# Kernel tuning notes

Hardware: AMD Instinct MI355X
Metric: run time of the kernel (lower is better)

The kernel has to match this reference:

```python
import jax, jax.numpy as jnp
import numpy as np

B, L, IN, H, E = 64, 255, 32, 256, 128
PAD = (L - 1) // 2
DN = ('NCH', 'OIH', 'NCH')


def setup_inputs() -> dict:
    ks = jax.random.split(jax.random.key(0), 10)
    r = lambda k, shp, s=0.05: jax.random.normal(k, shp, dtype=jnp.float32) * s
    return {
        's': jax.random.normal(ks[0], (B, L, IN), dtype=jnp.float32),
        'conv1_w': r(ks[1], (H, IN, L)),
        'conv1_b': r(ks[2], (H,)),
        'bn_gamma': jnp.ones((H,), jnp.float32),
        'bn_beta': jnp.zeros((H,), jnp.float32),
        'conv2_w': r(ks[3], (E, H, L)),
        'conv2_b': r(ks[4], (E,)),
        'pw1': r(ks[5], (E, H, L)),   # stacked Linear(L, H) weights, one per channel
        'pb1': r(ks[6], (E, H)),
        'pw2': r(ks[7], (E, 2, H)),   # stacked Linear(H, 2) weights
        'pb2': r(ks[8], (E, 2)),
    }


def reference(s, conv1_w, conv1_b, bn_gamma, bn_beta, conv2_w, conv2_b, pw1, pb1, pw2, pb2):
    x = jnp.transpose(s, (0, 2, 1))  # (B, IN, T)
    h = jax.lax.conv_general_dilated(x, conv1_w, (1,), [(PAD, PAD)], dimension_numbers=DN)
    h = jax.nn.relu(h + conv1_b[None, :, None])
    # BatchNorm1d in training mode: biased batch stats over (N, T)
    mean = h.mean(axis=(0, 2), keepdims=True)
    var = ((h - mean) ** 2).mean(axis=(0, 2), keepdims=True)
    h = (h - mean) * jax.lax.rsqrt(var + 1e-5) * bn_gamma[None, :, None] + bn_beta[None, :, None]
    z = jax.lax.conv_general_dilated(h, conv2_w, (1,), [(PAD, PAD)], dimension_numbers=DN)
    z = jnp.transpose(z + conv2_b[None, :, None], (0, 2, 1))  # (B, T, E)

    rf = jnp.fft.rfft(z, axis=1)                 # (B, F, E), F = L//2 + 1 == E
    power = jnp.abs(rf)[:, :, 1:] ** 2           # faithful channel-axis slice -> (B, F, E-1)
    freq_bins = jnp.fft.rfftfreq(L)[1:]          # (F-1,) == (E-1,)
    frequency = jnp.sum(freq_bins * power, axis=1) / jnp.sum(power, axis=1)  # (B, E-1)
    amplitude = 2.0 * jnp.sqrt(jnp.sum(power, axis=1)) / L                    # (B, E-1)
    offset = rf.real[:, :, 0] / L                                              # (B, E)

    # batched per-channel 2-layer MLP (replaces Python loop over embedding_dim)
    hmid = jax.nn.relu(jnp.einsum('btc,cht->bch', z, pw1) + pb1[None])  # (B, E, H)
    ang = jnp.einsum('bch,coh->bco', hmid, pw2) + pb2[None]             # (B, E, 2)
    phase = jnp.arctan2(ang[:, :, 1], ang[:, :, 0])                     # (B, E)
    return (amplitude, phase, frequency, offset)
```

## Files before the change

kernel.cpp:

```cpp
#include <hip/hip_runtime.h>
#include <math.h>

#define TB   64
#define TT   255
#define TIN  32
#define NH   256
#define NE   128
#define NK   255
#define NPAD 127

#define NF    384
#define NBINS 193
#define NFC   386
#define FCP   416
#define HCH   64

typedef __attribute__((ext_vector_type(8))) short short8;
typedef __attribute__((ext_vector_type(4))) float float4v;

#define WSB_WP1  0u
#define WSB_Z    0u
#define WSB_HFU  8388608u
#define WSB_HMID 8388608u
#define WSB_W2S  25165824u
#define WSB_HSP  37814272u
#define WSB_BIH  37814272u
#define WSB_BIL  38027264u
#define WSB_BIM  38240256u
#define WSB_ZSP  44138496u
#define WSB_BDH  56786944u
#define WSB_BDL  56984576u
#define WSB_BDM  57182208u
#define WSB_BWH  57379840u
#define WSB_BWL  57577472u
#define WSB_BWM  57775104u
#define WSB_D1   57972736u
#define WSB_BN   57974528u

#define O_AMP   0u
#define O_PHASE 8128u
#define O_FREQ  16320u
#define O_OFF   24448u

static __device__ __forceinline__ unsigned short f2bf(float f) {
  unsigned int u = __float_as_uint(f);
  unsigned int r = (u + 0x7FFFu + ((u >> 16) & 1u)) >> 16;
  return (unsigned short)r;
}
static __device__ __forceinline__ float bf2f(unsigned short s) {
  return __uint_as_float(((unsigned int)s) << 16);
}
static __device__ __forceinline__ short8 as_s8(uint4 v) {
  union { uint4 u; short8 s; } c; c.u = v; return c.s;
}

static __device__ __forceinline__ void split3(float x, unsigned short& h,
                                              unsigned short& l, unsigned short& m2) {
  h = f2bf(x);
  float r1 = x - bf2f(h);
  l = f2bf(r1);
// ... 41 lines not shown
  put_hi(U2, r, p, pm);
}
static __device__ __forceinline__ short8 frag(const unsigned short* __restrict__ lds,
                                              int row, int quad, int part) {
  return *(const short8*)&lds[row * 64 + (((quad ^ (part << 2)) ^ (row & 7)) << 3)];
}
#define MF(a, b, c) __builtin_amdgcn_mfma_f32_16x16x32_bf16((a), (b), (c), 0, 0, 0)
#define MF6(accv, ahv, alv, a2v, bhv, blv, b2v) do {                              \
    accv = MF(ahv, bhv, accv);                                                    \
    accv = MF(ahv, blv, accv);                                                    \
    accv = MF(alv, bhv, accv);                                                    \
    accv = MF(alv, blv, accv);                                                    \
    accv = MF(ahv, b2v, accv);                                                    \
    accv = MF(a2v, bhv, accv);                                                    \
  } while (0)
#define MF5(accv, ahv, alv, a2v, bhv, blv) do {                                   \
    accv = MF(ahv, bhv, accv);                                                    \
    accv = MF(ahv, blv, accv);                                                    \
    accv = MF(alv, bhv, accv);                                                    \
    accv = MF(alv, blv, accv);                                                    \
    accv = MF(a2v, bhv, accv);                                                    \
  } while (0)

__global__ __launch_bounds__(256) void bn_zero_k(float* __restrict__ bn) {
  bn[threadIdx.x] = 0.f;
  bn[256 + threadIdx.x] = 0.f;
}

__global__ __launch_bounds__(256) void basis_init_k(
    unsigned int* __restrict__ bdh, unsigned int* __restrict__ bdl,
    unsigned int* __restrict__ bdm, unsigned int* __restrict__ bwh,
    unsigned int* __restrict__ bwl, unsigned int* __restrict__ bwm) {
  __shared__ float sv[2][256];
  const int m = blockIdx.x;
  const int t = threadIdx.x;
  const int f = m >> 1, im = m & 1;
  const float C = 6.28318530717958647692f / 384.f;
  int r1 = (f * t) % 384;
  float th1 = C * (float)r1;
  sv[0][t] = (t == 255) ? 0.f : (im ? -sinf(th1) : cosf(th1));
  int a = f * (t - 127);
  int r2 = a % 384; if (r2 < 0) r2 += 384;
  float th2 = C * (float)r2;
  sv[1][t] = (t == 255) ? 0.f : (im ? sinf(th2) : cosf(th2));
  __syncthreads();
  const int which = t >> 7, j = t & 127;
  unsigned int ph, pl, pm;
  split_pack2(sv[which][2 * j], sv[which][2 * j + 1], ph, pl, pm);
  size_t off = (size_t)m * 128 + j;
  if (which == 0) { bdh[off] = ph; bdl[off] = pl; bdm[off] = pm; }
  else            { bwh[off] = ph; bwl[off] = pl; bwm[off] = pm; }
}

__global__ __launch_bounds__(256) void d1_k(float* __restrict__ d1) {
  const int fc = blockIdx.x * 256 + threadIdx.x;
  if (fc >= NFC) return;
  const int f = fc >> 1, im = fc & 1;
  const float C = 6.28318530717958647692f / 384.f;
  float s = 0.f;
  int r = 0;
  for (int t = 0; t < TT; ++t) {
    float th = C * (float)r;
    s += im ? -sinf(th) : cosf(th);
    r += f; if (r >= 384) r -= 384;
  }
  d1[fc] = s;
}

__global__ __launch_bounds__(256) void basis_bi_k(
    unsigned int* __restrict__ bih, unsigned int* __restrict__ bil,
    unsigned int* __restrict__ bim) {
  const int kp = blockIdx.x;
  const int t = threadIdx.x;
  float x0 = 0.f, x1 = 0.f;
  if (kp < NBINS) {
    const int f = kp;
    const float C = 6.28318530717958647692f / 384.f;
    int r1 = (f * t) % 384;
    float th = C * (float)r1;
    float wgt = ((f == 0 || f == 192) ? 1.f : 2.f) * (1.f / 384.f);
    x0 = cosf(th) * wgt;
    x1 = -sinf(th) * wgt;
  }
  unsigned int ph, pl, pm;
  split_pack2(x0, x1, ph, pl, pm);
  size_t off = (size_t)kp * 256 + t;
  bih[off] = ph; bil[off] = pl; bim[off] = pm;
}

__global__ __launch_bounds__(256) void pack1_k(const float* __restrict__ w1,
                                               unsigned int* __restrict__ wp1u) {
  __shared__ float tile[512][33];
  const int et = blockIdx.x, kc = blockIdx.y;
  const int kk0 = kc * 32, cnt = min(32, NK - kk0);
  const int tid = threadIdx.x;
  for (int idx = tid; idx < 512 * 32; idx += 256) {
    int row = idx >> 5, kl = idx & 31;
    if (kl < cnt) {
      int e_l = row >> 5, i_l = row & 31;
      tile[row][kl] = w1[(size_t)((et * 16 + e_l) * TIN + i_l) * NK + kk0 + kl];
    }
  }
  __syncthreads();
  const int lane = tid >> 2, jp = (tid & 3) * 2;
  const int row0 = (lane & 15) * 32 + (lane >> 4) * 8 + jp;
  for (int kl = 0; kl < cnt; ++kl) {
    float w0 = tile[row0][kl], w1v = tile[row0 + 1][kl];
    unsigned short h0 = f2bf(w0), h1 = f2bf(w1v);
    unsigned short l0 = f2bf(w0 - bf2f(h0)), l1 = f2bf(w1v - bf2f(h1));
    size_t base = (size_t)(kk0 + kl) * 8192 + et * 512 + tid;
    wp1u[base] = (unsigned int)h0 | ((unsigned int)h1 << 16);
    wp1u[base + 256] = (unsigned int)l0 | ((unsigned int)l1 << 16);
  }
}

#define C1_ROWS 384
__global__ __launch_bounds__(256, 2) void conv1_mfma(
    const float* __restrict__ s, const unsigned int* __restrict__ wp1u,
    const float* __restrict__ b1v, unsigned int* __restrict__ hfu,
    float* __restrict__ bn) {
  __shared__ __align__(16) unsigned short Alds[C1_ROWS * 64];
  const int th = blockIdx.x & 1, chg = blockIdx.x >> 1, b = blockIdx.y;
  const int tid = threadIdx.x, lane = tid & 63, wv = tid >> 6;
  const int quad = lane >> 4, l15 = lane & 15;
  const int tg = wv & 1, eg = wv >> 1;
  unsigned int* Au = (unsigned int*)Alds;

  for (int idx = tid; idx < C1_ROWS * 16; idx += 256) {
    int r = idx >> 4, p = idx & 15;
    int t = th * 128 + r - NPAD;
    float v0 = 0.f, v1 = 0.f;
    if (t >= 0 && t < TT) {
      const float* sp = &s[(size_t)(b * TT + t) * TIN + p * 2];
      v0 = sp[0]; v1 = sp[1];
    }
// ... 66 lines not shown
          unsigned short vh = f2bf(v);
          unsigned short vl = f2bf(v - bf2f(vh));
          hfu[(size_t)(b * 256 + t) * NH + ch] =
              (unsigned int)vh | ((unsigned int)vl << 16);
          s1[ni] += v; s2[ni] += v * v;
        }
      }
    }
  }
#pragma unroll
  for (int ni = 0; ni < 2; ++ni) {
    s1[ni] += __shfl_xor(s1[ni], 16);
    s1[ni] += __shfl_xor(s1[ni], 32);
    s2[ni] += __shfl_xor(s2[ni], 16);
    s2[ni] += __shfl_xor(s2[ni], 32);
    if (quad == 0) {
      int ch = chg * 64 + (eg * 2 + ni) * 16 + l15;
      atomicAdd(&bn[ch], s1[ni]);
      atomicAdd(&bn[256 + ch], s2[ni]);
    }
  }
#undef LOADB1
#undef MSTEP1
}

__global__ __launch_bounds__(256) void bn_final_k(const float* __restrict__ gamma,
                                                  const float* __restrict__ beta,
                                                  float* __restrict__ bn) {
  const int h = threadIdx.x;
  const float inv = 1.0f / (TB * TT);
  float m = bn[h] * inv;
  float var = bn[256 + h] * inv - m * m;
  float sc = gamma[h] / sqrtf(var + 1e-5f);
  bn[512 + h] = sc;
  bn[768 + h] = beta[h] - m * sc;
}


#define LOAD_A_PLANES(PH, PL, PM) do {                                            \
    if (fcA < NFC) {                                                              \
      size_t ab = (size_t)fcA * 128 + (k0 >> 1) + hfA * 8;                        \
      uint4 h0v = *(const uint4*)(PH + ab), h1v = *(const uint4*)(PH + ab + 4);   \
      uint4 l0v = *(const uint4*)(PL + ab), l1v = *(const uint4*)(PL + ab + 4);   \
      uint4 m0v = *(const uint4*)(PM + ab), m1v = *(const uint4*)(PM + ab + 4);   \
      _Pragma("unroll")                                                           \
      for (int q = 0; q < 4; ++q) {                                               \
        put_hi(Au, rA, hfA * 8 + q, ((const unsigned int*)&h0v)[q]);              \
        put_hi(Au, rA, hfA * 8 + 4 + q, ((const unsigned int*)&h1v)[q]);          \
        put_lo(Au, rA, hfA * 8 + q, ((const unsigned int*)&l0v)[q]);              \
        put_lo(Au, rA, hfA * 8 + 4 + q, ((const unsigned int*)&l1v)[q]);          \
        put_hi(A2u, rA, hfA * 8 + q, ((const unsigned int*)&m0v)[q]);             \
        put_hi(A2u, rA, hfA * 8 + 4 + q, ((const unsigned int*)&m1v)[q]);         \
      }                                                                           \
    } else {                                                                      \
      _Pragma("unroll")                                                           \
      for (int q = 0; q < 8; ++q) {                                               \
        put_hi(Au, rA, hfA * 8 + q, 0u);                                          \
        put_lo(Au, rA, hfA * 8 + q, 0u);                                          \
        put_hi(A2u, rA, hfA * 8 + q, 0u);                                         \
      }                                                                           \
    }                                                                             \
  } while (0)

__global__ __launch_bounds__(256, 2) void w2prep_mfma(
    const float* __restrict__ w2, const unsigned int* __restrict__ bwh,
    const unsigned int* __restrict__ bwl, const unsigned int* __restrict__ bwm,
    float* __restrict__ W, int h0c) {
  __shared__ __align__(16) unsigned short Alds[128 * 64];
  __shared__ __align__(16) unsigned short A2lds[128 * 64];
  __shared__ __align__(16) unsigned short Blds[128 * 64];
  __shared__ __align__(16) unsigned short B2lds[128 * 64];
  const int n0 = blockIdx.x * 128, m0 = blockIdx.y * 128;
  const int tid = threadIdx.x, lane = tid & 63, wv = tid >> 6;
  const int quad = lane >> 4, l15 = lane & 15;
  const int wm = wv >> 1, wn = wv & 1;
  unsigned int* Au = (unsigned int*)Alds;
  unsigned int* A2u = (unsigned int*)A2lds;
  unsigned int* Bu = (unsigned int*)Blds;
  unsigned int* B2u = (unsigned int*)B2lds;

  float4v acc[4][4];
#pragma unroll
  for (int i = 0; i < 4; ++i)
#pragma unroll
    for (int j = 0; j < 4; ++j) acc[i][j] = (float4v)(0.f);

  const int rA = tid >> 1, hfA = tid & 1;
  const int fcA = m0 + rA;
  const int lane8 = tid & 7, rsub = tid >> 3;

  for (int kk = 0; kk < 8; ++kk) {
    const int k0 = kk * 32;
    if (kk) __syncthreads();
    LOAD_A_PLANES(bwh, bwl, bwm);
#pragma unroll
    for (int pass = 0; pass < 4; ++pass) {
      int row = pass * 32 + rsub;
      int e = (n0 + row) >> 6, hl = (n0 + row) & 63;
      const float* src = w2 + ((size_t)(e * NH + h0c + hl)) * NK;
      int kb = k0 + lane8 * 4;
      float f0 = (kb < NK) ? src[kb] : 0.f;
      float f1 = (kb + 1 < NK) ? src[kb + 1] : 0.f;
      float f2 = (kb + 2 < NK) ? src[kb + 2] : 0.f;
      float f3 = (kb + 3 < NK) ? src[kb + 3] : 0.f;
      stage2_3(Bu, B2u, row, lane8 * 2, f0, f1);
      stage2_3(Bu, B2u, row, lane8 * 2 + 1, f2, f3);
    }
    __syncthreads();
    short8 bh[4], bl[4], b2[4];
#pragma unroll
    for (int ni = 0; ni < 4; ++ni) {
      int rb = wn * 64 + ni * 16 + l15;
      bh[ni] = frag(Blds, rb, quad, 0);
      bl[ni] = frag(Blds, rb, quad, 1);
      b2[ni] = frag(B2lds, rb, quad, 0);
    }
#pragma unroll
    for (int mi = 0; mi < 4; ++mi) {
      int ra = wm * 64 + mi * 16 + l15;
      short8 ah = frag(Alds, ra, quad, 0);
      short8 al = frag(Alds, ra, quad, 1);
      short8 a2 = frag(A2lds, ra, quad, 0);
#pragma unroll
      for (int ni = 0; ni < 4; ++ni) MF6(acc[mi][ni], ah, al, a2, bh[ni], bl[ni], b2[ni]);
    }
  }
#pragma unroll
  for (int mi = 0; mi < 4; ++mi) {
    int fc0 = m0 + wm * 64 + mi * 16 + quad * 4;
#pragma unroll
    for (int ni = 0; ni < 4; ++ni) {
      int n = n0 + wn * 64 + ni * 16 + l15;
#pragma unroll
      for (int r = 0; r < 4; ++r) {
        if (fc0 + r < NFC) W[(size_t)(fc0 + r) * 8192 + n] = acc[mi][ni][r];
      }
    }
  }
}

__global__ __launch_bounds__(256, 2) void dftH_mfma(
    const unsigned int* __restrict__ hfu, const float* __restrict__ bn,
    const unsigned int* __restrict__ bdh, const unsigned int* __restrict__ bdl,
    const unsigned int* __restrict__ bdm, const float* __restrict__ d1,
    float* __restrict__ H, int h0c) {
  __shared__ __align__(16) unsigned short Alds[128 * 64];
  __shared__ __align__(16) unsigned short A2lds[128 * 64];
  __shared__ __align__(16) unsigned short Blds[64 * 64];
  const int b = blockIdx.x, m0 = blockIdx.y * 128;
  const int tid = threadIdx.x, lane = tid & 63, wv = tid >> 6;
  const int quad = lane >> 4, l15 = lane & 15;
  const int wm = wv >> 1, wn = wv & 1;
  const int hl = tid & 63, g = tid >> 6;
  unsigned int* Au = (unsigned int*)Alds;
  unsigned int* A2u = (unsigned int*)A2lds;
  unsigned int* Bu = (unsigned int*)Blds;

  float4v acc[4][2];
#pragma unroll
  for (int i = 0; i < 4; ++i)
#pragma unroll
    for (int j = 0; j < 2; ++j) acc[i][j] = (float4v)(0.f);

  const int rA = tid >> 1, hfA = tid & 1;
  const int fcA = m0 + rA;

  for (int kk = 0; kk < 8; ++kk) {
    const int k0 = kk * 32;
    if (kk) __syncthreads();
    LOAD_A_PLANES(bdh, bdl, bdm);
#pragma unroll
    for (int j = 0; j < 4; ++j) {
      int tp = g * 4 + j;
      int t0 = k0 + tp * 2;
      unsigned int u0 = (t0 < TT)
          ? hfu[(size_t)(b * 256 + t0) * NH + h0c + hl] : 0u;
      unsigned int u1 = (t0 + 1 < TT)
          ? hfu[(size_t)(b * 256 + t0 + 1) * NH + h0c + hl] : 0u;
      unsigned int hp = (u0 & 0xFFFFu) | ((u1 & 0xFFFFu) << 16);
      unsigned int lp = (u0 >> 16) | (u1 & 0xFFFF0000u);
      put_hi(Bu, hl, tp, hp);
      put_lo(Bu, hl, tp, lp);
    }
    __syncthreads();
    short8 bh[2], bl[2];
#pragma unroll
    for (int ni = 0; ni < 2; ++ni) {
      int rb = wn * 32 + ni * 16 + l15;
      bh[ni] = frag(Blds, rb, quad, 0);
      bl[ni] = frag(Blds, rb, quad, 1);
    }
#pragma unroll
    for (int mi = 0; mi < 4; ++mi) {
      int ra = wm * 64 + mi * 16 + l15;
      short8 ah = frag(Alds, ra, quad, 0);
      short8 al = frag(Alds, ra, quad, 1);
      short8 a2 = frag(A2lds, ra, quad, 0);
#pragma unroll
      for (int ni = 0; ni < 2; ++ni) MF5(acc[mi][ni], ah, al, a2, bh[ni], bl[ni]);
    }
  }
#pragma unroll
  for (int mi = 0; mi < 4; ++mi) {
    int fc0 = m0 + wm * 64 + mi * 16 + quad * 4;
#pragma unroll
    for (int ni = 0; ni < 2; ++ni) {
      int hli = wn * 32 + ni * 16 + l15;
      float scv = bn[512 + h0c + hli];
      float shv = bn[768 + h0c + hli];
#pragma unroll
      for (int r = 0; r < 4; ++r) {
        int fc = fc0 + r;
        if (fc < NFC)
          H[(size_t)fc * 4096 + b * 64 + hli] = scv * acc[mi][ni][r] + shv * d1[fc];
      }
    }
  }
}

__global__ __launch_bounds__(256, 2) void fgemm_mfma(
    const float* __restrict__ H, const float* __restrict__ W,
    float* __restrict__ zsp, int first) {
  __shared__ __align__(16) unsigned short Alds[64 * 64];
  __shared__ __align__(16) unsigned short A2lds[64 * 64];
  __shared__ __align__(16) unsigned short Blds[128 * 64];
  __shared__ __align__(16) unsigned short B2lds[128 * 64];
  const int ri = blockIdx.x, f = blockIdx.y;
  const int tid = threadIdx.x, lane = tid & 63, wv = tid >> 6;
  const int quad = lane >> 4, l15 = lane & 15;
  const int wm = wv >> 1, wn = wv & 1;
  unsigned int* Au = (unsigned int*)Alds;
  unsigned int* A2u = (unsigned int*)A2lds;
  unsigned int* Bu = (unsigned int*)Blds;
  unsigned int* B2u = (unsigned int*)B2lds;

  float4v acc[2][4];
#pragma unroll
  for (int i = 0; i < 2; ++i)
#pragma unroll
    for (int j = 0; j < 4; ++j) acc[i][j] = (float4v)(0.f);

  const int rA = tid >> 2, qA = tid & 3;
  const int rB = tid >> 1, hB = tid & 1;

  for (int kk = 0; kk < 4; ++kk) {
    const int ca = kk >> 1;
    const int hb = (kk & 1) * 32;
    if (kk) __syncthreads();
    {
      float va[8];
      const float4* s4 = (const float4*)(H + (size_t)(2 * f + ca) * 4096 + rA * 64 + hb + qA * 8);
      *(float4*)(va + 0) = s4[0]; *(float4*)(va + 4) = s4[1];
      stage8_3(Au, A2u, rA, qA * 4, va);
    }
    {
      const int cb = ri ^ (kk >> 1);
      const int neg = (ri == 0 && kk >= 2);
      float vb[16];
      const float4* s4 = (const float4*)(W + (size_t)(2 * f + cb) * 8192 + rB * 64 + hb + hB * 16);
      *(float4*)(vb + 0) = s4[0]; *(float4*)(vb + 4) = s4[1];
      *(float4*)(vb + 8) = s4[2]; *(float4*)(vb + 12) = s4[3];
      if (neg) {
#pragma unroll
        for (int q = 0; q < 16; ++q) vb[q] = -vb[q];
      }
      stage8_3(Bu, B2u, rB, hB * 8, vb);
      stage8_3(Bu, B2u, rB, hB * 8 + 4, vb + 8);
    }
    __syncthreads();
    short8 bh[4], bl[4], b2[4];
#pragma unroll
    for (int ni = 0; ni < 4; ++ni) {
      int rb = wn * 64 + ni * 16 + l15;
      bh[ni] = frag(Blds, rb, quad, 0);
      bl[ni] = frag(Blds, rb, quad, 1);
      b2[ni] = frag(B2lds, rb, quad, 0);
    }
#pragma unroll
    for (int mi = 0; mi < 2; ++mi) {
      int ra = wm * 32 + mi * 16 + l15;
      short8 ah = frag(Alds, ra, quad, 0);
      short8 al = frag(Alds, ra, quad, 1);
      short8 a2 = frag(A2lds, ra, quad, 0);
#pragma unroll
      for (int ni = 0; ni < 4; ++ni) MF6(acc[mi][ni], ah, al, a2, bh[ni], bl[ni], b2[ni]);
    }
  }
  float* Z = zsp + (size_t)(2 * f + ri) * 8192;
#pragma unroll
  for (int mi = 0; mi < 2; ++mi) {
#pragma unroll
    for (int ni = 0; ni < 4; ++ni) {
      int e = wn * 64 + ni * 16 + l15;
#pragma unroll
      for (int r = 0; r < 4; ++r) {
        int b = wm * 32 + mi * 16 + quad * 4 + r;
        size_t off = (size_t)b * 128 + e;
        if (first) Z[off] = acc[mi][ni][r];
        else       Z[off] += acc[mi][ni][r];
      }
    }
  }
}

__global__ __launch_bounds__(256, 2) void idft_mfma(
    const float* __restrict__ zsp, const unsigned int* __restrict__ bih,
    const unsigned int* __restrict__ bil, const unsigned int* __restrict__ bim,
    const float* __restrict__ b2, float* __restrict__ z) {
  __shared__ __align__(16) unsigned short Alds[128 * 64];
  __shared__ __align__(16) unsigned short A2lds[128 * 64];
  __shared__ __align__(16) unsigned short Blds[64 * 64];
  __shared__ __align__(16) unsigned short B2lds[64 * 64];
  const int n0 = blockIdx.x * 64, m0 = blockIdx.y * 128;
  const int tid = threadIdx.x, lane = tid & 63, wv = tid >> 6;
  const int quad = lane >> 4, l15 = lane & 15;
  const int wm = wv >> 1, wn = wv & 1;
  const int tl = tid & 63, g = tid >> 6;
  unsigned int* Au = (unsigned int*)Alds;
  unsigned int* A2u = (unsigned int*)A2lds;
  unsigned int* Bu = (unsigned int*)Blds;
  unsigned int* B2u = (unsigned int*)B2lds;

  float4v acc[4][2];
#pragma unroll
  for (int i = 0; i < 4; ++i)
#pragma unroll
    for (int j = 0; j < 2; ++j) acc[i][j] = (float4v)(0.f);

  for (int kk = 0; kk < 13; ++kk) {
    const int k0 = kk * 32;
    if (kk) __syncthreads();
#pragma unroll
    for (int i = 0; i < 8; ++i) {
      int combo = i * 4 + g;
      int tp = combo >> 1, beh = combo & 1;
      int fc0 = k0 + tp * 2;
      int row = beh * 64 + lane;
      float v0 = (fc0 < NFC) ? zsp[(size_t)fc0 * 8192 + m0 + row] : 0.f;
      float v1 = (fc0 + 1 < NFC) ? zsp[(size_t)(fc0 + 1) * 8192 + m0 + row] : 0.f;
      stage2_3(Au, A2u, row, tp, v0, v1);
    }
#pragma unroll
    for (int j = 0; j < 4; ++j) {
      int tp = g * 4 + j;
      size_t off = (size_t)((k0 >> 1) + tp) * 256 + n0 + tl;
      put_hi(Bu, tl, tp, bih[off]);
      put_lo(Bu, tl, tp, bil[off]);
      put_hi(B2u, tl, tp, bim[off]);
    }
    __syncthreads();
    short8 bh[2], bl[2], b2f[2];
#pragma unroll
    for (int ni = 0; ni < 2; ++ni) {
      int rb = wn * 32 + ni * 16 + l15;
      bh[ni] = frag(Blds, rb, quad, 0);
      bl[ni] = frag(Blds, rb, quad, 1);
      b2f[ni] = frag(B2lds, rb, quad, 0);
    }
#pragma unroll
    for (int mi = 0; mi < 4; ++mi) {
      int ra = wm * 64 + mi * 16 + l15;
      short8 ah = frag(Alds, ra, quad, 0);
      short8 al = frag(Alds, ra, quad, 1);
      short8 a2 = frag(A2lds, ra, quad, 0);
#pragma unroll
      for (int ni = 0; ni < 2; ++ni) MF6(acc[mi][ni], ah, al, a2, bh[ni], bl[ni], b2f[ni]);
    }
  }
#pragma unroll
  for (int mi = 0; mi < 4; ++mi) {
#pragma unroll
// ... 35 lines not shown
      float4 zv = *(const float4*)&zl[t * 68 + b4 * 4];
      float4 pv = *(const float4*)&pl[t * 68 + h4 * 4];
      float zz[4] = {zv.x, zv.y, zv.z, zv.w};
      float pp[4] = {pv.x, pv.y, pv.z, pv.w};
#pragma unroll
      for (int a = 0; a < 4; ++a)
#pragma unroll
        for (int bb = 0; bb < 4; ++bb) acc[a][bb] = fmaf(pp[a], zz[bb], acc[a][bb]);
    }
  }
#pragma unroll
  for (int a = 0; a < 4; ++a) {
    int hh = h0 + h4 * 4 + a;
    float bias = pb1[c * NH + hh];
#pragma unroll
    for (int bb = 0; bb < 4; ++bb) {
      int bidx = b4 * 4 + bb;
      float v = acc[a][bb] + bias;
      hmid[(size_t)(bidx * NE + c) * NH + hh] = fmaxf(v, 0.f);
    }
  }
}

__global__ __launch_bounds__(256) void mlp2_k(const float* __restrict__ hmid,
                                              const float* __restrict__ pw2,
                                              const float* __restrict__ pb2,
                                              float* __restrict__ out) {
  const int tid = threadIdx.x, lane = tid & 63, wv = tid >> 6;
  const int p = blockIdx.x * 4 + wv;
  const int b = p >> 7, c = p & 127;
  const float4 hv = *(const float4*)&hmid[(size_t)(b * NE + c) * NH + lane * 4];
  const float4 p0 = *(const float4*)&pw2[(size_t)(c * 2 + 0) * NH + lane * 4];
  const float4 p1 = *(const float4*)&pw2[(size_t)(c * 2 + 1) * NH + lane * 4];
  float s0 = hv.x * p0.x + hv.y * p0.y + hv.z * p0.z + hv.w * p0.w;
  float s1 = hv.x * p1.x + hv.y * p1.y + hv.z * p1.z + hv.w * p1.w;
#pragma unroll
  for (int off = 32; off; off >>= 1) {
    s0 += __shfl_down(s0, off);
    s1 += __shfl_down(s1, off);
  }
  if (lane == 0) {
    float a0 = s0 + pb2[c * 2 + 0];
    float a1 = s1 + pb2[c * 2 + 1];
    out[O_PHASE + b * NE + c] = atan2f(a1, a0);
  }
}

__global__ __launch_bounds__(256) void amp_k(const float* __restrict__ z,
                                             float* __restrict__ out) {
  const int tid = threadIdx.x, lane = tid & 63, wv = tid >> 6;
  const int b = blockIdx.x, c = blockIdx.y * 4 + wv;
  const float* row = z + (size_t)(b * NE + c) * TT;
  float s1 = 0.f, s2 = 0.f;
  for (int idx = lane; idx < TT; idx += 64) {
    float v = row[idx];
    s1 += v; s2 += v * v;
  }
#pragma unroll
  for (int off = 32; off; off >>= 1) {
    s1 += __shfl_down(s1, off);
    s2 += __shfl_down(s2, off);
  }
  if (lane == 0 && c >= 1) {
    float P = 0.5f * (255.f * s2 + s1 * s1);
    out[O_AMP + b * 127 + (c - 1)] = 2.f * sqrtf(P) / 255.f;
    out[O_FREQ + b * 127 + (c - 1)] = (float)c / 255.f;
  }
}

__global__ __launch_bounds__(128) void offset_k(const float* __restrict__ z,
                                                float* __restrict__ out) {
  __shared__ float zr[TT];
  __shared__ float ct[TT];
  const int b = blockIdx.x, tid = threadIdx.x;
  for (int idx = tid; idx < TT; idx += 128) {
    zr[idx] = z[(size_t)(b * NE + 0) * TT + idx];
    ct[idx] = cosf(6.283185307179586f * (float)idx / 255.f);
  }
  __syncthreads();
  const int f = tid;
  float s = 0.f;
  int m = 0;
  for (int t = 0; t < TT; ++t) {
    s += zr[t] * ct[m];
    m += f; if (m >= TT) m -= TT;
  }
  out[O_OFF + b * NE + f] = s / 255.f;
}

extern "C" void kernel_launch(void* const* d_in, const int* in_sizes, int n_in,
                              void* d_out, int out_size, void* d_ws, size_t ws_size,
                              hipStream_t stream) {
  (void)in_sizes; (void)n_in; (void)out_size; (void)ws_size;
  const float* s       = (const float*)d_in[0];
  const float* conv1_w = (const float*)d_in[1];
  const float* conv1_b = (const float*)d_in[2];
  const float* bn_g    = (const float*)d_in[3];
  const float* bn_b    = (const float*)d_in[4];
  const float* conv2_w = (const float*)d_in[5];
  const float* conv2_b = (const float*)d_in[6];
  const float* pw1     = (const float*)d_in[7];
  const float* pb1     = (const float*)d_in[8];
  const float* pw2     = (const float*)d_in[9];
  const float* pb2     = (const float*)d_in[10];
  float* out = (float*)d_out;
  char* ws   = (char*)d_ws;

  unsigned int* wp1u = (unsigned int*)(ws + WSB_WP1);
  float* z    = (float*)(ws + WSB_Z);
  unsigned int* hfu = (unsigned int*)(ws + WSB_HFU);
  float* hmid = (float*)(ws + WSB_HMID);
  float* W2s  = (float*)(ws + WSB_W2S);
  float* Hs   = (float*)(ws + WSB_HSP);
  float* zsp  = (float*)(ws + WSB_ZSP);
  unsigned int* bdh = (unsigned int*)(ws + WSB_BDH);
  unsigned int* bdl = (unsigned int*)(ws + WSB_BDL);
  unsigned int* bdm = (unsigned int*)(ws + WSB_BDM);
  unsigned int* bwh = (unsigned int*)(ws + WSB_BWH);
  unsigned int* bwl = (unsigned int*)(ws + WSB_BWL);
  unsigned int* bwm = (unsigned int*)(ws + WSB_BWM);
  unsigned int* bih = (unsigned int*)(ws + WSB_BIH);
  unsigned int* bil = (unsigned int*)(ws + WSB_BIL);
  unsigned int* bim = (unsigned int*)(ws + WSB_BIM);
  float* d1 = (float*)(ws + WSB_D1);
  float* bn = (float*)(ws + WSB_BN);

  bn_zero_k<<<1, 256, 0, stream>>>(bn);
  basis_init_k<<<NFC, 256, 0, stream>>>(bdh, bdl, bdm, bwh, bwl, bwm);
  d1_k<<<2, 256, 0, stream>>>(d1);
  pack1_k<<<dim3(16, 8), 256, 0, stream>>>(conv1_w, wp1u);

  conv1_mfma<<<dim3(8, TB), 256, 0, stream>>>(s, wp1u, conv1_b, hfu, bn);
  bn_final_k<<<1, 256, 0, stream>>>(bn_g, bn_b, bn);

  for (int c = 0; c < 4; ++c) {
    w2prep_mfma<<<dim3(64, 4), 256, 0, stream>>>(conv2_w, bwh, bwl, bwm, W2s, c * HCH);
    dftH_mfma<<<dim3(64, 4), 256, 0, stream>>>(hfu, bn, bdh, bdl, bdm, d1, Hs, c * HCH);
    fgemm_mfma<<<dim3(2, NBINS), 256, 0, stream>>>(Hs, W2s, zsp, c == 0 ? 1 : 0);
  }
  basis_bi_k<<<208, 256, 0, stream>>>(bih, bil, bim);
  idft_mfma<<<dim3(4, 64), 256, 0, stream>>>(zsp, bih, bil, bim, conv2_b, z);

  mlp1_k<<<dim3(4, NE), 256, 0, stream>>>(z, pw1, pb1, hmid);
  mlp2_k<<<TB * NE / 4, 256, 0, stream>>>(hmid, pw2, pb2, out);
  amp_k<<<dim3(TB, 32), 256, 0, stream>>>(z, out);
  offset_k<<<TB, 128, 0, stream>>>(z, out);
}
```

Baseline: 729.4 us.

## Merge setup and tail kernels, run DFT-H once, rechunk the conv2 frequency GEMM

Folds the init kernels (bn zero, basis, d1, weight packing) into one launch and the three output kernels into one tail kernel. The BN finalize step moves into dftH, which now runs once over all 256 channels into a larger H buffer instead of four times. The w2prep/fgemm loop drops from four 64-channel chunks to three chunks of 96/96/64. The inverse-DFT basis is rebuilt on the fly from the forward basis planes, so its separate init kernel goes away. Launch count falls, at the cost of a bigger workspace and a non-power-of-two index split.

```diff
diff --git a/kernel.cpp b/kernel.cpp
--- a/kernel.cpp
+++ b/kernel.cpp
@@ -13,29 +13,26 @@
 #define NBINS 193
 #define NFC   386
 #define FCP   416
-#define HCH   64
+#define W2ROW 12288
+#define HSROW 16384
 
 typedef __attribute__((ext_vector_type(8))) short short8;
 typedef __attribute__((ext_vector_type(4))) float float4v;
 
-#define WSB_WP1  0u
+#define WSB_W2S  0u
 #define WSB_Z    0u
 #define WSB_HFU  8388608u
 #define WSB_HMID 8388608u
-#define WSB_W2S  25165824u
-#define WSB_HSP  37814272u
-#define WSB_BIH  37814272u
-#define WSB_BIL  38027264u
-#define WSB_BIM  38240256u
-#define WSB_ZSP  44138496u
-#define WSB_BDH  56786944u
-#define WSB_BDL  56984576u
-#define WSB_BDM  57182208u
-#define WSB_BWH  57379840u
-#define WSB_BWL  57577472u
-#define WSB_BWM  57775104u
-#define WSB_D1   57972736u
-#define WSB_BN   57974528u
+#define WSB_ZSP  18972672u
+#define WSB_HS   31621120u
+#define WSB_BDH  56918144u
+#define WSB_BDL  57115776u
+#define WSB_BDM  57313408u
+#define WSB_BWH  57511040u
+#define WSB_BWL  57708672u
+#define WSB_BWM  57906304u
+#define WSB_D1   58103936u
+#define WSB_BN   58105984u
 
 #define O_AMP   0u
 #define O_PHASE 8128u
@@ -123,95 +120,77 @@
     accv = MF(a2v, bhv, accv);                                                    \
   } while (0)
 
-__global__ __launch_bounds__(256) void bn_zero_k(float* __restrict__ bn) {
-  bn[threadIdx.x] = 0.f;
-  bn[256 + threadIdx.x] = 0.f;
-}
-
-__global__ __launch_bounds__(256) void basis_init_k(
+__global__ __launch_bounds__(256) void init_k(
+    const float* __restrict__ w1, unsigned int* __restrict__ wp1u,
     unsigned int* __restrict__ bdh, unsigned int* __restrict__ bdl,
     unsigned int* __restrict__ bdm, unsigned int* __restrict__ bwh,
-    unsigned int* __restrict__ bwl, unsigned int* __restrict__ bwm) {
-  __shared__ float sv[2][256];
-  const int m = blockIdx.x;
-  const int t = threadIdx.x;
-  const int f = m >> 1, im = m & 1;
-  const float C = 6.28318530717958647692f / 384.f;
-  int r1 = (f * t) % 384;
-  float th1 = C * (float)r1;
-  sv[0][t] = (t == 255) ? 0.f : (im ? -sinf(th1) : cosf(th1));
-  int a = f * (t - 127);
-  int r2 = a % 384; if (r2 < 0) r2 += 384;
-  float th2 = C * (float)r2;
-  sv[1][t] = (t == 255) ? 0.f : (im ? sinf(th2) : cosf(th2));
-  __syncthreads();
-  const int which = t >> 7, j = t & 127;
-  unsigned int ph, pl, pm;
-  split_pack2(sv[which][2 * j], sv[which][2 * j + 1], ph, pl, pm);
-  size_t off = (size_t)m * 128 + j;
-  if (which == 0) { bdh[off] = ph; bdl[off] = pl; bdm[off] = pm; }
-  else            { bwh[off] = ph; bwl[off] = pl; bwm[off] = pm; }
-}
-
-__global__ __launch_bounds__(256) void d1_k(float* __restrict__ d1) {
-  const int fc = blockIdx.x * 256 + threadIdx.x;
-  if (fc >= NFC) return;
-  const int f = fc >> 1, im = fc & 1;
-  const float C = 6.28318530717958647692f / 384.f;
-  float s = 0.f;
-  int r = 0;
-  for (int t = 0; t < TT; ++t) {
-    float th = C * (float)r;
-    s += im ? -sinf(th) : cosf(th);
-    r += f; if (r >= 384) r -= 384;
-  }
-  d1[fc] = s;
-}
-
-__global__ __launch_bounds__(256) void basis_bi_k(
-    unsigned int* __restrict__ bih, unsigned int* __restrict__ bil,
-    unsigned int* __restrict__ bim) {
-  const int kp = blockIdx.x;
-  const int t = threadIdx.x;
-  float x0 = 0.f, x1 = 0.f;
-  if (kp < NBINS) {
-    const int f = kp;
+    unsigned int* __restrict__ bwl, unsigned int* __restrict__ bwm,
+    float* __restrict__ d1, float* __restrict__ bn) {
+  __shared__ float tile[512][33];
+  const int bid = blockIdx.x, tid = threadIdx.x;
+  if (bid == 0) {
+    bn[tid] = 0.f;
+    bn[256 + tid] = 0.f;
+    return;
+  }
+  if (bid < 387) {
+    float* sv = (float*)tile;
+    const int m = bid - 1, t = tid;
+    const int f = m >> 1, im = m & 1;
     const float C = 6.28318530717958647692f / 384.f;
     int r1 = (f * t) % 384;
-    float th = C * (float)r1;
-    float wgt = ((f == 0 || f == 192) ? 1.f : 2.f) * (1.f / 384.f);
-    x0 = cosf(th) * wgt;
-    x1 = -sinf(th) * wgt;
-  }
-  unsigned int ph, pl, pm;
-  split_pack2(x0, x1, ph, pl, pm);
-  size_t off = (size_t)kp * 256 + t;
-  bih[off] = ph; bil[off] = pl; bim[off] = pm;
-}
-
-__global__ __launch_bounds__(256) void pack1_k(const float* __restrict__ w1,
-                                               unsigned int* __restrict__ wp1u) {
-  __shared__ float tile[512][33];
-  const int et = blockIdx.x, kc = blockIdx.y;
-  const int kk0 = kc * 32, cnt = min(32, NK - kk0);
-  const int tid = threadIdx.x;
-  for (int idx = tid; idx < 512 * 32; idx += 256) {
-    int row = idx >> 5, kl = idx & 31;
-    if (kl < cnt) {
-      int e_l = row >> 5, i_l = row & 31;
-      tile[row][kl] = w1[(size_t)((et * 16 + e_l) * TIN + i_l) * NK + kk0 + kl];
-    }
-  }
-  __syncthreads();
-  const int lane = tid >> 2, jp = (tid & 3) * 2;
-  const int row0 = (lane & 15) * 32 + (lane >> 4) * 8 + jp;
-  for (int kl = 0; kl < cnt; ++kl) {
-    float w0 = tile[row0][kl], w1v = tile[row0 + 1][kl];
-    unsigned short h0 = f2bf(w0), h1 = f2bf(w1v);
-    unsigned short l0 = f2bf(w0 - bf2f(h0)), l1 = f2bf(w1v - bf2f(h1));
-    size_t base = (size_t)(kk0 + kl) * 8192 + et * 512 + tid;
-    wp1u[base] = (unsigned int)h0 | ((unsigned int)h1 << 16);
-    wp1u[base + 256] = (unsigned int)l0 | ((unsigned int)l1 << 16);
+    float th1 = C * (float)r1;
+    sv[t] = (t == 255) ? 0.f : (im ? -sinf(th1) : cosf(th1));
+    int a = f * (t - 127);
+    int r2 = a % 384; if (r2 < 0) r2 += 384;
+    float th2 = C * (float)r2;
+    sv[256 + t] = (t == 255) ? 0.f : (im ? sinf(th2) : cosf(th2));
+    __syncthreads();
+    const int which = t >> 7, j = t & 127;
+    unsigned int ph, pl, pm;
+    split_pack2(sv[which * 256 + 2 * j], sv[which * 256 + 2 * j + 1], ph, pl, pm);
+    size_t off = (size_t)m * 128 + j;
+    if (which == 0) { bdh[off] = ph; bdl[off] = pl; bdm[off] = pm; }
+    else            { bwh[off] = ph; bwl[off] = pl; bwm[off] = pm; }
+    return;
+  }
+  if (bid < 389) {
+    const int fc = (bid - 387) * 256 + tid;
+    if (fc >= NFC) return;
+    const int f = fc >> 1, im = fc & 1;
+    const float C = 6.28318530717958647692f / 384.f;
+    float s = 0.f;
+    int r = 0;
+    for (int t = 0; t < TT; ++t) {
+      float th = C * (float)r;
+      s += im ? -sinf(th) : cosf(th);
+      r += f; if (r >= 384) r -= 384;
+    }
+    d1[fc] = s;
+    return;
+  }
+  {
+    const int q = bid - 389;
+    const int et = q >> 3, kc = q & 7;
+    const int kk0 = kc * 32, cnt = min(32, NK - kk0);
+    for (int idx = tid; idx < 512 * 32; idx += 256) {
+      int row = idx >> 5, kl = idx & 31;
+      if (kl < cnt) {
+        int e_l = row >> 5, i_l = row & 31;
+        tile[row][kl] = w1[(size_t)((et * 16 + e_l) * TIN + i_l) * NK + kk0 + kl];
+      }
+    }
+    __syncthreads();
+    const int lane = tid >> 2, jp = (tid & 3) * 2;
+    const int row0 = (lane & 15) * 32 + (lane >> 4) * 8 + jp;
+    for (int kl = 0; kl < cnt; ++kl) {
+      float w0 = tile[row0][kl], w1v = tile[row0 + 1][kl];
+      unsigned short h0 = f2bf(w0), h1 = f2bf(w1v);
+      unsigned short l0 = f2bf(w0 - bf2f(h0)), l1 = f2bf(w1v - bf2f(h1));
+      size_t base = (size_t)(kk0 + kl) * 8192 + et * 512 + tid;
+      wp1u[base] = (unsigned int)h0 | ((unsigned int)h1 << 16);
+      wp1u[base + 256] = (unsigned int)l0 | ((unsigned int)l1 << 16);
+    }
   }
 }
 
@@ -324,18 +303,6 @@
   }
 #undef LOADB1
 #undef MSTEP1
-}
-
-__global__ __launch_bounds__(256) void bn_final_k(const float* __restrict__ gamma,
-                                                  const float* __restrict__ beta,
-                                                  float* __restrict__ bn) {
-  const int h = threadIdx.x;
-  const float inv = 1.0f / (TB * TT);
-  float m = bn[h] * inv;
-  float var = bn[256 + h] * inv - m * m;
-  float sc = gamma[h] / sqrtf(var + 1e-5f);
-  bn[512 + h] = sc;
-  bn[768 + h] = beta[h] - m * sc;
 }
 
 
@@ -364,10 +331,102 @@
     }                                                                             \
   } while (0)
 
+__global__ __launch_bounds__(256, 2) void dftH_mfma(
+    const unsigned int* __restrict__ hfu, const float* __restrict__ bn,
+    const float* __restrict__ gamma, const float* __restrict__ beta,
+    const unsigned int* __restrict__ bdh, const unsigned int* __restrict__ bdl,
+    const unsigned int* __restrict__ bdm, const float* __restrict__ d1,
+    float* __restrict__ H) {
+  __shared__ __align__(16) unsigned short Alds[128 * 64];
+  __shared__ __align__(16) unsigned short A2lds[128 * 64];
+  __shared__ __align__(16) unsigned short Blds[64 * 64];
+  __shared__ float scs[64], shs[64];
+  const int b = blockIdx.x, m0 = blockIdx.y * 128, h0c = blockIdx.z * 64;
+  const int tid = threadIdx.x, lane = tid & 63, wv = tid >> 6;
+  const int quad = lane >> 4, l15 = lane & 15;
+  const int wm = wv >> 1, wn = wv & 1;
+  const int hl = tid & 63, g = tid >> 6;
+  unsigned int* Au = (unsigned int*)Alds;
+  unsigned int* A2u = (unsigned int*)A2lds;
+  unsigned int* Bu = (unsigned int*)Blds;
+
+  if (tid < 64) {
+    int h = h0c + tid;
+    const float inv = 1.0f / (TB * TT);
+    float m = bn[h] * inv;
+    float var = bn[256 + h] * inv - m * m;
+    float sc = gamma[h] / sqrtf(var + 1e-5f);
+    scs[tid] = sc;
+    shs[tid] = beta[h] - m * sc;
+  }
+
+  float4v acc[4][2];
+#pragma unroll
+  for (int i = 0; i < 4; ++i)
+#pragma unroll
+    for (int j = 0; j < 2; ++j) acc[i][j] = (float4v)(0.f);
+
+  const int rA = tid >> 1, hfA = tid & 1;
+  const int fcA = m0 + rA;
+
+  for (int kk = 0; kk < 8; ++kk) {
+    const int k0 = kk * 32;
+    if (kk) __syncthreads();
+    LOAD_A_PLANES(bdh, bdl, bdm);
+#pragma unroll
+    for (int j = 0; j < 4; ++j) {
+      int tp = g * 4 + j;
+      int t0 = k0 + tp * 2;
+      unsigned int u0 = (t0 < TT)
+          ? hfu[(size_t)(b * 256 + t0) * NH + h0c + hl] : 0u;
+      unsigned int u1 = (t0 + 1 < TT)
+          ? hfu[(size_t)(b * 256 + t0 + 1) * NH + h0c + hl] : 0u;
+      unsigned int hp = (u0 & 0xFFFFu) | ((u1 & 0xFFFFu) << 16);
+      unsigned int lp = (u0 >> 16) | (u1 & 0xFFFF0000u);
+      put_hi(Bu, hl, tp, hp);
+      put_lo(Bu, hl, tp, lp);
+    }
+    __syncthreads();
+    short8 bh[2], bl[2];
+#pragma unroll
+    for (int ni = 0; ni < 2; ++ni) {
+      int rb = wn * 32 + ni * 16 + l15;
+      bh[ni] = frag(Blds, rb, quad, 0);
+      bl[ni] = frag(Blds, rb, quad, 1);
+    }
+#pragma unroll
+    for (int mi = 0; mi < 4; ++mi) {
+      int ra = wm * 64 + mi * 16 + l15;
+      short8 ah = frag(Alds, ra, quad, 0);
+      short8 al = frag(Alds, ra, quad, 1);
+      short8 a2 = frag(A2lds, ra, quad, 0);
+#pragma unroll
+      for (int ni = 0; ni < 2; ++ni) MF5(acc[mi][ni], ah, al, a2, bh[ni], bl[ni]);
+    }
+  }
+#pragma unroll
+  for (int mi = 0; mi < 4; ++mi) {
+    int fc0 = m0 + wm * 64 + mi * 16 + quad * 4;
+#pragma unroll
+    for (int ni = 0; ni < 2; ++ni) {
+      int hli = wn * 32 + ni * 16 + l15;
+      float scv = scs[hli];
+      float shv = shs[hli];
+#pragma unroll
+      for (int r = 0; r < 4; ++r) {
+        int fc = fc0 + r;
+        if (fc < NFC)
+          H[(size_t)fc * HSROW + b * 256 + h0c + hli] =
+              scv * acc[mi][ni][r] + shv * d1[fc];
+      }
+    }
+  }
+}
+
 __global__ __launch_bounds__(256, 2) void w2prep_mfma(
     const float* __restrict__ w2, const unsigned int* __restrict__ bwh,
     const unsigned int* __restrict__ bwl, const unsigned int* __restrict__ bwm,
-    float* __restrict__ W, int h0c) {
+    float* __restrict__ W, int h0c, int hcnt) {
   __shared__ __align__(16) unsigned short Alds[128 * 64];
   __shared__ __align__(16) unsigned short A2lds[128 * 64];
   __shared__ __align__(16) unsigned short Blds[128 * 64];
@@ -398,13 +457,15 @@
 #pragma unroll
     for (int pass = 0; pass < 4; ++pass) {
       int row = pass * 32 + rsub;
-      int e = (n0 + row) >> 6, hl = (n0 + row) & 63;
+      int n = n0 + row;
+      int e = n / 96, hl = n - e * 96;
+      int ok = (hl < hcnt);
       const float* src = w2 + ((size_t)(e * NH + h0c + hl)) * NK;
       int kb = k0 + lane8 * 4;
-      float f0 = (kb < NK) ? src[kb] : 0.f;
-      float f1 = (kb + 1 < NK) ? src[kb + 1] : 0.f;
-      float f2 = (kb + 2 < NK) ? src[kb + 2] : 0.f;
-      float f3 = (kb + 3 < NK) ? src[kb + 3] : 0.f;
+      float f0 = (ok && kb < NK) ? src[kb] : 0.f;
+      float f1 = (ok && kb + 1 < NK) ? src[kb + 1] : 0.f;
+      float f2 = (ok && kb + 2 < NK) ? src[kb + 2] : 0.f;
+      float f3 = (ok && kb + 3 < NK) ? src[kb + 3] : 0.f;
       stage2_3(Bu, B2u, row, lane8 * 2, f0, f1);
       stage2_3(Bu, B2u, row, lane8 * 2 + 1, f2, f3);
     }
@@ -435,86 +496,7 @@
       int n = n0 + wn * 64 + ni * 16 + l15;
 #pragma unroll
       for (int r = 0; r < 4; ++r) {
-        if (fc0 + r < NFC) W[(size_t)(fc0 + r) * 8192 + n] = acc[mi][ni][r];
-      }
-    }
-  }
-}
-
-__global__ __launch_bounds__(256, 2) void dftH_mfma(
-    const unsigned int* __restrict__ hfu, const float* __restrict__ bn,
-    const unsigned int* __restrict__ bdh, const unsigned int* __restrict__ bdl,
-    const unsigned int* __restrict__ bdm, const float* __restrict__ d1,
-    float* __restrict__ H, int h0c) {
-  __shared__ __align__(16) unsigned short Alds[128 * 64];
-  __shared__ __align__(16) unsigned short A2lds[128 * 64];
-  __shared__ __align__(16) unsigned short Blds[64 * 64];
-  const int b = blockIdx.x, m0 = blockIdx.y * 128;
-  const int tid = threadIdx.x, lane = tid & 63, wv = tid >> 6;
-  const int quad = lane >> 4, l15 = lane & 15;
-  const int wm = wv >> 1, wn = wv & 1;
-  const int hl = tid & 63, g = tid >> 6;
-  unsigned int* Au = (unsigned int*)Alds;
-  unsigned int* A2u = (unsigned int*)A2lds;
-  unsigned int* Bu = (unsigned int*)Blds;
-
-  float4v acc[4][2];
-#pragma unroll
-  for (int i = 0; i < 4; ++i)
-#pragma unroll
-    for (int j = 0; j < 2; ++j) acc[i][j] = (float4v)(0.f);
-
-  const int rA = tid >> 1, hfA = tid & 1;
-  const int fcA = m0 + rA;
-
-  for (int kk = 0; kk < 8; ++kk) {
-    const int k0 = kk * 32;
-    if (kk) __syncthreads();
-    LOAD_A_PLANES(bdh, bdl, bdm);
-#pragma unroll
-    for (int j = 0; j < 4; ++j) {
-      int tp = g * 4 + j;
-      int t0 = k0 + tp * 2;
-      unsigned int u0 = (t0 < TT)
-          ? hfu[(size_t)(b * 256 + t0) * NH + h0c + hl] : 0u;
-      unsigned int u1 = (t0 + 1 < TT)
-          ? hfu[(size_t)(b * 256 + t0 + 1) * NH + h0c + hl] : 0u;
-      unsigned int hp = (u0 & 0xFFFFu) | ((u1 & 0xFFFFu) << 16);
-      unsigned int lp = (u0 >> 16) | (u1 & 0xFFFF0000u);
-      put_hi(Bu, hl, tp, hp);
-      put_lo(Bu, hl, tp, lp);
-    }
-    __syncthreads();
-    short8 bh[2], bl[2];
-#pragma unroll
-    for (int ni = 0; ni < 2; ++ni) {
-      int rb = wn * 32 + ni * 16 + l15;
-      bh[ni] = frag(Blds, rb, quad, 0);
-      bl[ni] = frag(Blds, rb, quad, 1);
-    }
-#pragma unroll
-    for (int mi = 0; mi < 4; ++mi) {
-      int ra = wm * 64 + mi * 16 + l15;
-      short8 ah = frag(Alds, ra, quad, 0);
-      short8 al = frag(Alds, ra, quad, 1);
-      short8 a2 = frag(A2lds, ra, quad, 0);
-#pragma unroll
-      for (int ni = 0; ni < 2; ++ni) MF5(acc[mi][ni], ah, al, a2, bh[ni], bl[ni]);
-    }
-  }
-#pragma unroll
-  for (int mi = 0; mi < 4; ++mi) {
-    int fc0 = m0 + wm * 64 + mi * 16 + quad * 4;
-#pragma unroll
-    for (int ni = 0; ni < 2; ++ni) {
-      int hli = wn * 32 + ni * 16 + l15;
-      float scv = bn[512 + h0c + hli];
-      float shv = bn[768 + h0c + hli];
-#pragma unroll
-      for (int r = 0; r < 4; ++r) {
-        int fc = fc0 + r;
-        if (fc < NFC)
-          H[(size_t)fc * 4096 + b * 64 + hli] = scv * acc[mi][ni][r] + shv * d1[fc];
+        if (fc0 + r < NFC) W[(size_t)(fc0 + r) * W2ROW + n] = acc[mi][ni][r];
       }
     }
   }
@@ -522,7 +504,7 @@
 
 __global__ __launch_bounds__(256, 2) void fgemm_mfma(
     const float* __restrict__ H, const float* __restrict__ W,
-    float* __restrict__ zsp, int first) {
+    float* __restrict__ zsp, int c96, int nks, int first) {
   __shared__ __align__(16) unsigned short Alds[64 * 64];
   __shared__ __align__(16) unsigned short A2lds[64 * 64];
   __shared__ __align__(16) unsigned short Blds[128 * 64];
@@ -545,21 +527,23 @@
   const int rA = tid >> 2, qA = tid & 3;
   const int rB = tid >> 1, hB = tid & 1;
 
-  for (int kk = 0; kk < 4; ++kk) {
-    const int ca = kk >> 1;
-    const int hb = (kk & 1) * 32;
-    if (kk) __syncthreads();
+  for (int ph = 0; ph < 2 * nks; ++ph) {
+    const int ca = (ph >= nks) ? 1 : 0;
+    const int hsub = (ph - ca * nks) * 32;
+    if (ph) __syncthreads();
     {
       float va[8];
-      const float4* s4 = (const float4*)(H + (size_t)(2 * f + ca) * 4096 + rA * 64 + hb + qA * 8);
+      const float4* s4 = (const float4*)(H + (size_t)(2 * f + ca) * HSROW +
+                                         rA * 256 + c96 + hsub + qA * 8);
       *(float4*)(va + 0) = s4[0]; *(float4*)(va + 4) = s4[1];
       stage8_3(Au, A2u, rA, qA * 4, va);
     }
     {
-      const int cb = ri ^ (kk >> 1);
-      const int neg = (ri == 0 && kk >= 2);
+      const int cb = ri ^ ca;
+      const int neg = (ri == 0 && ca == 1);
       float vb[16];
-      const float4* s4 = (const float4*)(W + (size_t)(2 * f + cb) * 8192 + rB * 64 + hb + hB * 16);
+      const float4* s4 = (const float4*)(W + (size_t)(2 * f + cb) * W2ROW +
+                                         rB * 96 + hsub + hB * 16);
       *(float4*)(vb + 0) = s4[0]; *(float4*)(vb + 4) = s4[1];
       *(float4*)(vb + 8) = s4[2]; *(float4*)(vb + 12) = s4[3];
       if (neg) {
@@ -606,8 +590,8 @@
 }
 
 __global__ __launch_bounds__(256, 2) void idft_mfma(
-    const float* __restrict__ zsp, const unsigned int* __restrict__ bih,
-    const unsigned int* __restrict__ bil, const unsigned int* __restrict__ bim,
+    const float* __restrict__ zsp, const unsigned int* __restrict__ bdh,
+    const unsigned int* __restrict__ bdl, const unsigned int* __restrict__ bdm,
     const float* __restrict__ b2, float* __restrict__ z) {
   __shared__ __align__(16) unsigned short Alds[128 * 64];
   __shared__ __align__(16) unsigned short A2lds[128 * 64];
@@ -645,10 +629,22 @@
 #pragma unroll
     for (int j = 0; j < 4; ++j) {
       int tp = g * 4 + j;
-      size_t off = (size_t)((k0 >> 1) + tp) * 256 + n0 + tl;
-      put_hi(Bu, tl, tp, bih[off]);
-      put_lo(Bu, tl, tp, bil[off]);
-      put_hi(B2u, tl, tp, bim[off]);
+      int fc0 = k0 + tp * 2;
+      float x0 = 0.f, x1 = 0.f;
+      if (fc0 < NFC) {
+        int fq = fc0 >> 1;
+        float sw = ((fq == 0 || fq == 192) ? 1.f : 2.f) * (1.f / 384.f);
+        int t = n0 + tl;
+        int pi = t >> 1, hs = (t & 1) * 16;
+        size_t o0 = (size_t)fc0 * 128 + pi, o1 = o0 + 128;
+        x0 = (bf2f((unsigned short)(bdh[o0] >> hs)) +
+              bf2f((unsigned short)(bdl[o0] >> hs)) +
+              bf2f((unsigned short)(bdm[o0] >> hs))) * sw;
+        x1 = (bf2f((unsigned short)(bdh[o1] >> hs)) +
+              bf2f((unsigned short)(bdl[o1] >> hs)) +
+              bf2f((unsigned short)(bdm[o1] >> hs))) * sw;
+      }
+      stage2_3(Bu, B2u, tl, tp, x0, x1);
     }
     __syncthreads();
     short8 bh[2], bl[2], b2f[2];
@@ -730,70 +726,74 @@
   }
 }
 
-__global__ __launch_bounds__(256) void mlp2_k(const float* __restrict__ hmid,
+__global__ __launch_bounds__(256) void tail_k(const float* __restrict__ hmid,
                                               const float* __restrict__ pw2,
                                               const float* __restrict__ pb2,
+                                              const float* __restrict__ z,
                                               float* __restrict__ out) {
-  const int tid = threadIdx.x, lane = tid & 63, wv = tid >> 6;
-  const int p = blockIdx.x * 4 + wv;
-  const int b = p >> 7, c = p & 127;
-  const float4 hv = *(const float4*)&hmid[(size_t)(b * NE + c) * NH + lane * 4];
-  const float4 p0 = *(const float4*)&pw2[(size_t)(c * 2 + 0) * NH + lane * 4];
-  const float4 p1 = *(const float4*)&pw2[(size_t)(c * 2 + 1) * NH + lane * 4];
-  float s0 = hv.x * p0.x + hv.y * p0.y + hv.z * p0.z + hv.w * p0.w;
-  float s1 = hv.x * p1.x + hv.y * p1.y + hv.z * p1.z + hv.w * p1.w;
-#pragma unroll
-  for (int off = 32; off; off >>= 1) {
-    s0 += __shfl_down(s0, off);
-    s1 += __shfl_down(s1, off);
-  }
-  if (lane == 0) {
-    float a0 = s0 + pb2[c * 2 + 0];
-    float a1 = s1 + pb2[c * 2 + 1];
-    out[O_PHASE + b * NE + c] = atan2f(a1, a0);
-  }
-}
-
-__global__ __launch_bounds__(256) void amp_k(const float* __restrict__ z,
-                                             float* __restrict__ out) {
-  const int tid = threadIdx.x, lane = tid & 63, wv = tid >> 6;
-  const int b = blockIdx.x, c = blockIdx.y * 4 + wv;
-  const float* row = z + (size_t)(b * NE + c) * TT;
-  float s1 = 0.f, s2 = 0.f;
-  for (int idx = lane; idx < TT; idx += 64) {
-    float v = row[idx];
-    s1 += v; s2 += v * v;
-  }
-#pragma unroll
-  for (int off = 32; off; off >>= 1) {
-    s1 += __shfl_down(s1, off);
-    s2 += __shfl_down(s2, off);
-  }
-  if (lane == 0 && c >= 1) {
-    float P = 0.5f * (255.f * s2 + s1 * s1);
-    out[O_AMP + b * 127 + (c - 1)] = 2.f * sqrtf(P) / 255.f;
-    out[O_FREQ + b * 127 + (c - 1)] = (float)c / 255.f;
-  }
-}
-
-__global__ __launch_bounds__(128) void offset_k(const float* __restrict__ z,
-                                                float* __restrict__ out) {
   __shared__ float zr[TT];
   __shared__ float ct[TT];
-  const int b = blockIdx.x, tid = threadIdx.x;
-  for (int idx = tid; idx < TT; idx += 128) {
-    zr[idx] = z[(size_t)(b * NE + 0) * TT + idx];
-    ct[idx] = cosf(6.283185307179586f * (float)idx / 255.f);
-  }
-  __syncthreads();
-  const int f = tid;
-  float s = 0.f;
-  int m = 0;
-  for (int t = 0; t < TT; ++t) {
-    s += zr[t] * ct[m];
-    m += f; if (m >= TT) m -= TT;
-  }
-  out[O_OFF + b * NE + f] = s / 255.f;
+  const int bid = blockIdx.x, tid = threadIdx.x;
+  const int lane = tid & 63, wv = tid >> 6;
+  if (bid < 2048) {
+    const int p = bid * 4 + wv;
+    const int b = p >> 7, c = p & 127;
+    const float4 hv = *(const float4*)&hmid[(size_t)(b * NE + c) * NH + lane * 4];
+    const float4 p0 = *(const float4*)&pw2[(size_t)(c * 2 + 0) * NH + lane * 4];
+    const float4 p1 = *(const float4*)&pw2[(size_t)(c * 2 + 1) * NH + lane * 4];
+    float s0 = hv.x * p0.x + hv.y * p0.y + hv.z * p0.z + hv.w * p0.w;
+    float s1 = hv.x * p1.x + hv.y * p1.y + hv.z * p1.z + hv.w * p1.w;
+#pragma unroll
+    for (int off = 32; off; off >>= 1) {
+      s0 += __shfl_down(s0, off);
+      s1 += __shfl_down(s1, off);
+    }
+    if (lane == 0) {
+      float a0 = s0 + pb2[c * 2 + 0];
+      float a1 = s1 + pb2[c * 2 + 1];
+      out[O_PHASE + b * NE + c] = atan2f(a1, a0);
+    }
+    return;
+  }
+  if (bid < 4096) {
+    const int q = bid - 2048;
+    const int b = q >> 5, c = (q & 31) * 4 + wv;
+    const float* row = z + (size_t)(b * NE + c) * TT;
+    float s1 = 0.f, s2 = 0.f;
+    for (int idx = lane; idx < TT; idx += 64) {
+      float v = row[idx];
+      s1 += v; s2 += v * v;
+    }
+#pragma unroll
+    for (int off = 32; off; off >>= 1) {
+      s1 += __shfl_down(s1, off);
+      s2 += __shfl_down(s2, off);
+    }
+    if (lane == 0 && c >= 1) {
+      float P = 0.5f * (255.f * s2 + s1 * s1);
+      out[O_AMP + b * 127 + (c - 1)] = 2.f * sqrtf(P) / 255.f;
+      out[O_FREQ + b * 127 + (c - 1)] = (float)c / 255.f;
+    }
+    return;
+  }
+  {
+    const int b = bid - 4096;
+    for (int idx = tid; idx < TT; idx += 256) {
+      zr[idx] = z[(size_t)(b * NE + 0) * TT + idx];
+      ct[idx] = cosf(6.283185307179586f * (float)idx / 255.f);
+    }
+    __syncthreads();
+    if (tid < 128) {
+      const int f = tid;
+      float s = 0.f;
+      int m = 0;
+      for (int t = 0; t < TT; ++t) {
+        s += zr[t] * ct[m];
+        m += f; if (m >= TT) m -= TT;
+      }
+      out[O_OFF + b * NE + f] = s / 255.f;
+    }
+  }
 }
 
 extern "C" void kernel_launch(void* const* d_in, const int* in_sizes, int n_in,
@@ -814,12 +814,12 @@
   float* out = (float*)d_out;
   char* ws   = (char*)d_ws;
 
-  unsigned int* wp1u = (unsigned int*)(ws + WSB_WP1);
+  unsigned int* wp1u = (unsigned int*)(ws + WSB_W2S);
   float* z    = (float*)(ws + WSB_Z);
   unsigned int* hfu = (unsigned int*)(ws + WSB_HFU);
   float* hmid = (float*)(ws + WSB_HMID);
   float* W2s  = (float*)(ws + WSB_W2S);
-  float* Hs   = (float*)(ws + WSB_HSP);
+  float* Hs   = (float*)(ws + WSB_HS);
   float* zsp  = (float*)(ws + WSB_ZSP);
   unsigned int* bdh = (unsigned int*)(ws + WSB_BDH);
   unsigned int* bdl = (unsigned int*)(ws + WSB_BDL);
@@ -827,30 +827,23 @@
   unsigned int* bwh = (unsigned int*)(ws + WSB_BWH);
   unsigned int* bwl = (unsigned int*)(ws + WSB_BWL);
   unsigned int* bwm = (unsigned int*)(ws + WSB_BWM);
-  unsigned int* bih = (unsigned int*)(ws + WSB_BIH);
-  unsigned int* bil = (unsigned int*)(ws + WSB_BIL);
-  unsigned int* bim = (unsigned int*)(ws + WSB_BIM);
   float* d1 = (float*)(ws + WSB_D1);
   float* bn = (float*)(ws + WSB_BN);
 
-  bn_zero_k<<<1, 256, 0, stream>>>(bn);
-  basis_init_k<<<NFC, 256, 0, stream>>>(bdh, bdl, bdm, bwh, bwl, bwm);
-  d1_k<<<2, 256, 0, stream>>>(d1);
-  pack1_k<<<dim3(16, 8), 256, 0, stream>>>(conv1_w, wp1u);
-
+  init_k<<<517, 256, 0, stream>>>(conv1_w, wp1u, bdh, bdl, bdm, bwh, bwl, bwm, d1, bn);
   conv1_mfma<<<dim3(8, TB), 256, 0, stream>>>(s, wp1u, conv1_b, hfu, bn);
-  bn_final_k<<<1, 256, 0, stream>>>(bn_g, bn_b, bn);
-
-  for (int c = 0; c < 4; ++c) {
-    w2prep_mfma<<<dim3(64, 4), 256, 0, stream>>>(conv2_w, bwh, bwl, bwm, W2s, c * HCH);
-    dftH_mfma<<<dim3(64, 4), 256, 0, stream>>>(hfu, bn, bdh, bdl, bdm, d1, Hs, c * HCH);
-    fgemm_mfma<<<dim3(2, NBINS), 256, 0, stream>>>(Hs, W2s, zsp, c == 0 ? 1 : 0);
-  }
-  basis_bi_k<<<208, 256, 0, stream>>>(bih, bil, bim);
-  idft_mfma<<<dim3(4, 64), 256, 0, stream>>>(zsp, bih, bil, bim, conv2_b, z);
-
+  dftH_mfma<<<dim3(64, 4, 4), 256, 0, stream>>>(hfu, bn, bn_g, bn_b,
+                                                bdh, bdl, bdm, d1, Hs);
+  const int h0cs[3] = {0, 96, 192};
+  const int hcnts[3] = {96, 96, 64};
+  const int nkss[3] = {3, 3, 2};
+  for (int c = 0; c < 3; ++c) {
+    w2prep_mfma<<<dim3(96, 4), 256, 0, stream>>>(conv2_w, bwh, bwl, bwm, W2s,
+                                                 h0cs[c], hcnts[c]);
+    fgemm_mfma<<<dim3(2, NBINS), 256, 0, stream>>>(Hs, W2s, zsp,
+                                                   h0cs[c], nkss[c], c == 0 ? 1 : 0);
+  }
+  idft_mfma<<<dim3(4, 64), 256, 0, stream>>>(zsp, bdh, bdl, bdm, conv2_b, z);
   mlp1_k<<<dim3(4, NE), 256, 0, stream>>>(z, pw1, pb1, hmid);
-  mlp2_k<<<TB * NE / 4, 256, 0, stream>>>(hmid, pw2, pb2, out);
-  amp_k<<<dim3(TB, 32), 256, 0, stream>>>(z, out);
-  offset_k<<<TB, 128, 0, stream>>>(z, out);
-}
+  tail_k<<<4160, 256, 0, stream>>>(hmid, pw2, pb2, z, out);
+}
```

New measurement: 628.3 us. 1.16x faster.
